# Performance work log

Hardware: AMD Instinct MI355X
Metric: run time of the kernel (lower is better)

Reference implementation:

```python
import jax, jax.numpy as jnp
import numpy as np

# Episode / graph constants
B, N, K, Q = 16, 5, 5, 5              # episodes, ways, shots, queries-per-class
NPG = 200                              # nodes per graph
DEG = 16                               # avg degree
F_DIM, H_DIM, OUT_DIM = 128, 128, 64
NS_G = B * N * K                       # 400 support graphs
NQ_G = B * N * Q                       # 400 query graphs
NS_NODES = NS_G * NPG                  # 80000
NQ_NODES = NQ_G * NPG                  # 80000
NEG_SLOPE = 0.2


def _rand_edges(key, n_nodes):
    # random in-graph source per (dst, k) slot; dst covers every node DEG times
    n_edges = n_nodes * DEG
    off = (jnp.arange(n_edges) // (NPG * DEG)) * NPG
    src = jax.random.randint(key, (n_edges,), 0, NPG) + off
    dst = jnp.repeat(jnp.arange(n_nodes), DEG)
    return jnp.stack([src, dst]).astype(jnp.int64)


def setup_inputs() -> dict:
    key = jax.random.key(0)
    ks = jax.random.split(key, 16)
    g = lambda k, shape, scale: jax.random.normal(k, shape, jnp.float32) * scale
    inp = {
        "supports_x": g(ks[0], (NS_NODES, F_DIM), 1.0),
        "queries_x": g(ks[1], (NQ_NODES, F_DIM), 1.0),
        "supports_edge_index": _rand_edges(ks[2], NS_NODES),
        "queries_edge_index": _rand_edges(ks[3], NQ_NODES),
        "supports_batch": (jnp.arange(NS_NODES) // NPG).astype(jnp.int64),
        "queries_batch": (jnp.arange(NQ_NODES) // NPG).astype(jnp.int64),
        # per-episode labels: N classes, K graphs each, local class ids 0..N-1
        "supports_y": jnp.tile(jnp.repeat(jnp.arange(N), K), B).astype(jnp.int64),
        "W1": g(ks[4], (F_DIM, H_DIM), 1.0 / np.sqrt(F_DIM)),
        "a1_src": g(ks[5], (H_DIM,), 1.0 / np.sqrt(H_DIM)),
        "a1_dst": g(ks[6], (H_DIM,), 1.0 / np.sqrt(H_DIM)),
        "b1": jnp.zeros((H_DIM,), jnp.float32),
        "W2": g(ks[7], (H_DIM, H_DIM), 1.0 / np.sqrt(H_DIM)),
        "a2_src": g(ks[8], (H_DIM,), 1.0 / np.sqrt(H_DIM)),
        "a2_dst": g(ks[9], (H_DIM,), 1.0 / np.sqrt(H_DIM)),
        "b2": jnp.zeros((H_DIM,), jnp.float32),
        "Wm1": g(ks[10], (H_DIM, H_DIM), 1.0 / np.sqrt(H_DIM)),
        "bm1": jnp.zeros((H_DIM,), jnp.float32),
        "Wm2": g(ks[11], (H_DIM, OUT_DIM), 1.0 / np.sqrt(H_DIM)),
        "bm2": jnp.zeros((OUT_DIM,), jnp.float32),
    }
    return inp


def gat_conv(x, src, dst, W, a_src, a_dst, b, n_nodes):
    """PyG GATConv, heads=1, add_self_loops=True."""
    xw = x @ W                                        # [n, H]
    loop = jnp.arange(n_nodes)
    src2 = jnp.concatenate([src, loop])
    dst2 = jnp.concatenate([dst, loop])
    e = (xw @ a_src)[src2] + (xw @ a_dst)[dst2]       # [E+n]
    e = jnp.where(e > 0, e, NEG_SLOPE * e)            # leaky_relu
    m = jax.ops.segment_max(e, dst2, num_segments=n_nodes)
    ex = jnp.exp(e - m[dst2])
    den = jax.ops.segment_sum(ex, dst2, num_segments=n_nodes)
    alpha = ex / den[dst2]                            # softmax per destination
    out = jax.ops.segment_sum(alpha[:, None] * xw[src2], dst2, num_segments=n_nodes)
    return out + b


def embed(x, edge_index, batch, n_graphs, W1, a1s, a1d, b1, W2, a2s, a2d, b2,
          Wm1, bm1, Wm2, bm2):
    n = x.shape[0]
    src, dst = edge_index[0], edge_index[1]
    h = jax.nn.relu(gat_conv(x, src, dst, W1, a1s, a1d, b1, n))
    h = jax.nn.relu(gat_conv(h, src, dst, W2, a2s, a2d, b2, n))
    h = jax.nn.relu(h @ Wm1 + bm1) @ Wm2 + bm2        # MLP
    # global mean pool
    s = jax.ops.segment_sum(h, batch, num_segments=n_graphs)
    cnt = jax.ops.segment_sum(jnp.ones((n,), h.dtype), batch, num_segments=n_graphs)
    return s / cnt[:, None]                           # [n_graphs, OUT_DIM]


def reference(supports_x, supports_edge_index, supports_batch, supports_y,
              queries_x, queries_edge_index, queries_batch,
              W1, a1_src, a1_dst, b1, W2, a2_src, a2_dst, b2,
              Wm1, bm1, Wm2, bm2):
    params = (W1, a1_src, a1_dst, b1, W2, a2_src, a2_dst, b2, Wm1, bm1, Wm2, bm2)
    emb_s = embed(supports_x, supports_edge_index, supports_batch, NS_G, *params)
    emb_q = embed(queries_x, queries_edge_index, queries_batch, NQ_G, *params)

    # class prototypes per episode: mean of supports with each (sorted) class label
    emb_s = emb_s.reshape(B, N * K, OUT_DIM)
    y = supports_y.reshape(B, N * K)
    onehot = jax.nn.one_hot(y, N, dtype=emb_s.dtype)          # [B, NK, N]
    proto = jnp.einsum("bkn,bke->bne", onehot, emb_s)
    proto = proto / onehot.sum(axis=1)[:, :, None]            # [B, N, E]

    # align queries with prototypes
    nq = N * Q                                                # queries per episode
    emb_q = emb_q.reshape(B, nq, OUT_DIM)
    rep_q = jnp.repeat(emb_q, N, axis=1)                      # repeat_interleave
    rep_p = jnp.tile(proto, (1, nq, 1))                       # repeat
    return rep_q.reshape(B * nq * N, OUT_DIM), rep_p.reshape(B * nq * N, OUT_DIM)
```

## Files before the change

kernel.cpp:

```cpp
#include <hip/hip_runtime.h>


typedef unsigned short u16;
typedef unsigned int   u32;
typedef unsigned char  u8;
typedef __attribute__((ext_vector_type(8))) short short8;
typedef __attribute__((ext_vector_type(4))) float f32x4;

#define NNODES   80000
#define DEG      16
#define NEDGES   (NNODES * DEG)
#define NGRAPH   400
#define NPG      200
#define FDIM     128
#define ODIM     64
#define NEPS     16
#define NWAY     5
#define NSHOT    5
#define NROWS    (2 * NNODES)
#define NGR2     (2 * NGRAPH)

__device__ __forceinline__ float b2f(u16 u) {
    return __uint_as_float(((u32)u) << 16);
}
__device__ __forceinline__ u16 f2b(float f) {
    u32 i = __float_as_uint(f);
    u32 r = i + 0x7FFFu + ((i >> 16) & 1u);
    return (u16)(r >> 16);
}

__global__ void detect_kernel(const u32* __restrict__ sx,
                              const int* __restrict__ ei,
                              int* __restrict__ flags)
{
    if (blockIdx.x == 0 && threadIdx.x == 0) {
        int ok32 = (ei[NEDGES + 16000] == 1000) && (ei[NEDGES + 32000] == 2000);
        flags[0] = ok32 ? 0 : 1;
        int cnt = 0;
        for (int i = 0; i < 64; i++) {
            u32 lo = sx[i] & 0xFFFFu;
            u32 e  = (lo >> 7) & 0xFFu;
            if (e >= 110u && e <= 135u) cnt++;
        }
        flags[1] = (cnt >= 32) ? 1 : 0;
    }
}

__global__ __launch_bounds__(256)
void canon_kernel(const void* __restrict__ W1, const void* __restrict__ W2,
                  const void* __restrict__ Wm1, const void* __restrict__ Wm2,
                  const void* a1s, const void* a1d, const void* b1,
                  const void* a2s, const void* a2d, const void* b2,
                  const void* bm1, const void* bm2,
                  const int* __restrict__ flags, u16* __restrict__ Wc,
                  float* __restrict__ Vc, float* __restrict__ emb)
{
    const int b = blockIdx.x, t = threadIdx.x;
    const int isb = flags[1];
    if (b < 224) {
        int idx = b * 256 + t;
        const void* src;
        int n, k, nout;
        if (idx < 16384)      { src = W1;  int l = idx;         n = l >> 7; k = l & 127; nout = 128; }
        else if (idx < 32768) { src = W2;  int l = idx - 16384; n = l >> 7; k = l & 127; nout = 128; }
        else if (idx < 49152) { src = Wm1; int l = idx - 32768; n = l >> 7; k = l & 127; nout = 128; }
        else                  { src = Wm2; int l = idx - 49152; n = l >> 7; k = l & 127; nout = 64; }
        int off = k * nout + n;
        Wc[idx] = isb ? ((const u16*)src)[off] : f2b(((const float*)src)[off]);
    } else if (b == 224) {
        for (int idx = t; idx < 960; idx += 256) {
            int g = idx >> 7, off = idx & 127;
            const void* src = (g == 0) ? a1s : (g == 1) ? a1d : (g == 2) ? b1 :
                              (g == 3) ? a2s : (g == 4) ? a2d : (g == 5) ? b2 :
                              (g == 6) ? bm1 : bm2;
            Vc[idx] = isb ? b2f(((const u16*)src)[off]) : ((const float*)src)[off];
        }
    } else {
        int i = (b - 225) * 256 + t;
        emb[i] = 0.f;
    }
}

__global__ __launch_bounds__(512)
void gemm_pack_kernel(const void* __restrict__ in0, const void* __restrict__ in1,
                      int in_mode, const int* __restrict__ flags,
                      const u16* __restrict__ Wt, const float* __restrict__ bias,
                      const float* __restrict__ avs, const float* __restrict__ avd,
                      u32* __restrict__ outP, float* __restrict__ es_g,
                      float* __restrict__ ed_g, int do_relu)
{
    __shared__ uint4 bsh[2048];

    const int t    = threadIdx.x;
    const int wv   = t >> 6;
    const int lane = t & 63;
    const int qd   = lane >> 4, md = lane & 15;

    int mode = in_mode;
    if (mode == 2) mode = flags[1];

    const size_t rowG = (size_t)blockIdx.x * 128 + wv * 16 + md;
    const int side = rowG >= NNODES;
    const size_t lrow = rowG - (side ? NNODES : 0);
    const void* in_ = side ? in1 : in0;

    short8 afr[4];
    if (mode) {
        const short* arow = (const short*)in_ + lrow * FDIM;
#pragma unroll
        for (int ks = 0; ks < 4; ks++)
            afr[ks] = *(const short8*)(arow + ks * 32 + qd * 8);
    } else {
        const float* arow = (const float*)in_ + lrow * FDIM;
#pragma unroll
        for (int ks = 0; ks < 4; ks++) {
            float4 u = *(const float4*)(arow + ks * 32 + qd * 8);
            float4 v = *(const float4*)(arow + ks * 32 + qd * 8 + 4);
            short8 tt;
            tt[0] = (short)f2b(u.x); tt[1] = (short)f2b(u.y);
            tt[2] = (short)f2b(u.z); tt[3] = (short)f2b(u.w);
            tt[4] = (short)f2b(v.x); tt[5] = (short)f2b(v.y);
            tt[6] = (short)f2b(v.z); tt[7] = (short)f2b(v.w);
            afr[ks] = tt;
        }
    }

    {
        const uint4* w4 = (const uint4*)Wt;
#pragma unroll
        for (int it = 0; it < 4; ++it) {
            int u   = it * 512 + t;
            int ctb = u >> 8, mdb = (u >> 4) & 15, ksb = (u >> 2) & 3, qdb = u & 3;
            bsh[ctb * 256 + ksb * 64 + qdb * 16 + mdb] = w4[u];
        }
    }
    __syncthreads();

    const size_t r0 = (size_t)blockIdx.x * 128 + wv * 16 + qd * 4;
    const bool has_av = (avs != nullptr);

    float sv[4] = {0.f, 0.f, 0.f, 0.f};
    float dv[4] = {0.f, 0.f, 0.f, 0.f};

    for (int ct = 0; ct < 8; ct++) {
        f32x4 acc = {0.f, 0.f, 0.f, 0.f};
#pragma unroll
        for (int ks = 0; ks < 4; ks++) {
            short8 bfr = *(const short8*)&bsh[(ct * 4 + ks) * 64 + lane];
            acc = __builtin_amdgcn_mfma_f32_16x16x32_bf16(afr[ks], bfr, acc, 0, 0, 0);
        }
        const int col = ct * 16 + md;
        const float bv  = bias ? bias[col] : 0.f;
        const float asv = has_av ? avs[col] : 0.f;
        const float adv = has_av ? avd[col] : 0.f;
#pragma unroll
        for (int i = 0; i < 4; i++) {
            float v = acc[i] + bv;
            if (do_relu) v = fmaxf(v, 0.f);
            sv[i] = fmaf(v, asv, sv[i]);
            dv[i] = fmaf(v, adv, dv[i]);
            float pr = __shfl_xor(v, 1, 64);
            if (!(md & 1)) {
                u32 pk = (u32)f2b(v) | ((u32)f2b(pr) << 16);
                outP[(r0 + i) * 64 + ct * 8 + (md >> 1)] = pk;
            }
        }
    }

    if (has_av) {
#pragma unroll
        for (int off = 1; off <= 8; off <<= 1) {
#pragma unroll
            for (int i = 0; i < 4; i++) {
                sv[i] += __shfl_xor(sv[i], off, 64);
                dv[i] += __shfl_xor(dv[i], off, 64);
            }
        }
        if (md == 0) {
#pragma unroll
            for (int i = 0; i < 4; i++) {
                es_g[r0 + i] = sv[i];
                ed_g[r0 + i] = dv[i];
            }
        }
    }
}

__global__ __launch_bounds__(512)
void gemm_pool_kernel(const u32* __restrict__ inP, const u16* __restrict__ Wt,
                      float* __restrict__ emb)
{
    __shared__ uint4 bsh[1024];
    __shared__ float psum[2][8][64];

    const int t = threadIdx.x;
    const int wv   = t >> 6;
    const int lane = t & 63;
    const int qd   = lane >> 4, md = lane & 15;

    const size_t rowA = (size_t)blockIdx.x * 128 + wv * 16 + md;
    const short* arow = (const short*)inP + rowA * FDIM;
    short8 afr[4];
#pragma unroll
    for (int ks = 0; ks < 4; ks++)
        afr[ks] = *(const short8*)(arow + ks * 32 + qd * 8);

    {
        const uint4* w4 = (const uint4*)Wt;
#pragma unroll
        for (int it = 0; it < 2; ++it) {
            int u   = it * 512 + t;
            int ctb = u >> 8, mdb = (u >> 4) & 15, ksb = (u >> 2) & 3, qdb = u & 3;
            bsh[ctb * 256 + ksb * 64 + qdb * 16 + mdb] = w4[u];
        }
    }
    __syncthreads();

    const int r0       = blockIdx.x * 128 + wv * 16 + qd * 4;
    const int g0       = (blockIdx.x * 128) / NPG;
    const int boundary = (g0 + 1) * NPG;

    for (int ct = 0; ct < 4; ct++) {
        f32x4 acc = {0.f, 0.f, 0.f, 0.f};
#pragma unroll
        for (int ks = 0; ks < 4; ks++) {
            short8 bfr = *(const short8*)&bsh[(ct * 4 + ks) * 64 + lane];
            acc = __builtin_amdgcn_mfma_f32_16x16x32_bf16(afr[ks], bfr, acc, 0, 0, 0);
        }
        float s0 = 0.f, s1 = 0.f;
#pragma unroll
        for (int i = 0; i < 4; i++) {
            if (r0 + i >= boundary) s1 += acc[i];
            else                    s0 += acc[i];
        }
        s0 += __shfl_xor(s0, 16, 64);  s1 += __shfl_xor(s1, 16, 64);
        s0 += __shfl_xor(s0, 32, 64);  s1 += __shfl_xor(s1, 32, 64);
        if (qd == 0) {
            psum[0][wv][ct * 16 + md] = s0;
            psum[1][wv][ct * 16 + md] = s1;
        }
    }
    __syncthreads();

    if (t < 128) {
        int p = t >> 6, c = t & 63;
        float s = 0.f;
#pragma unroll
        for (int w = 0; w < 8; w++) s += psum[p][w][c];
        if (p == 0 || boundary < blockIdx.x * 128 + 128)
            atomicAdd(&emb[(size_t)(g0 + p) * ODIM + c], s * (1.f / (float)NPG));
    }
}

__global__ __launch_bounds__(1024)
void gat_kernel(const u32* __restrict__ xwP, const float* __restrict__ es_g,
                const float* __restrict__ ed_g, const int* __restrict__ src0,
                const int* __restrict__ src1, const int* __restrict__ flags,
                const float* __restrict__ bias, u32* __restrict__ outH)
{
    __shared__ u32 xls[NPG * 64];
    __shared__ u16 alA[NPG * 18];
    __shared__ u8  slA[NPG * 20];

    const int g = blockIdx.x, t = threadIdx.x;
    const int side  = g >= NGRAPH;
    const int gbase = g * NPG;
    const int lbase = (g - (side ? NGRAPH : 0)) * NPG;
    const int* __restrict__ src = side ? src1 : src0;

    for (int idx = t; idx < NPG * 64; idx += 1024)
        xls[idx] = xwP[(size_t)gbase * 64 + idx];

    if (t < NPG) {
        const int n = t;
        const int is64 = flags[0];
        const float edn = ed_g[gbase + n];
        int sl[17];
#pragma unroll
        for (int j = 0; j < 16; j++) {
            int eidx = (lbase + n) * DEG + j;
            int sg = is64 ? src[2 * eidx] : src[eidx];
            sl[j] = sg - lbase;
        }
        sl[16] = n;
        float e[17];
        float mx = -1e30f;
#pragma unroll
        for (int j = 0; j < 17; j++) {
            float ev = es_g[gbase + sl[j]] + edn;
            ev = (ev > 0.f) ? ev : 0.2f * ev;
            e[j] = ev;
            mx = fmaxf(mx, ev);
        }
        float den = 0.f;
#pragma unroll
        for (int j = 0; j < 17; j++) {
            e[j] = __expf(e[j] - mx);
            den += e[j];
        }
        const float inv = 65535.f / den;
#pragma unroll
        for (int j = 0; j < 17; j++) {
            alA[n * 18 + j] = (u16)(e[j] * inv + 0.5f);
            slA[n * 20 + j] = (u8)sl[j];
        }
    }
    __syncthreads();

    const int w = t >> 6, l = t & 63;
    const int half = l >> 5, li = l & 31;
    const float4 bz = *(const float4*)&bias[4 * li];

    for (int p = w; p < NPG / 2; p += 16) {
        const int n = 2 * p + half;
        float h0 = 0.f, h1 = 0.f, h2 = 0.f, h3 = 0.f;
#pragma unroll
        for (int j = 0; j < 17; j++) {
            float a = (float)alA[n * 18 + j] * (1.f / 65535.f);
            int   s = (int)slA[n * 20 + j];
            uint2 q = *(const uint2*)&xls[s * 64 + 2 * li];
            h0 = fmaf(a, __uint_as_float(q.x << 16), h0);
            h1 = fmaf(a, __uint_as_float(q.x & 0xFFFF0000u), h1);
            h2 = fmaf(a, __uint_as_float(q.y << 16), h2);
            h3 = fmaf(a, __uint_as_float(q.y & 0xFFFF0000u), h3);
        }
        h0 = fmaxf(h0 + bz.x, 0.f);
        h1 = fmaxf(h1 + bz.y, 0.f);
        h2 = fmaxf(h2 + bz.z, 0.f);
        h3 = fmaxf(h3 + bz.w, 0.f);
        uint2 o;
        o.x = (u32)f2b(h0) | ((u32)f2b(h1) << 16);
        o.y = (u32)f2b(h2) | ((u32)f2b(h3) << 16);
        *(uint2*)&outH[(size_t)(gbase + n) * 64 + 2 * li] = o;
    }
}

__global__ __launch_bounds__(256)
void expand_kernel(const float* __restrict__ emb, const float* __restrict__ bm2,
                   const int* __restrict__ flags, void* __restrict__ out)
{
    int idx = blockIdx.x * 256 + threadIdx.x;
    const int TOT = NEPS * 125 * ODIM;
    if (idx >= TOT) return;
    int c = idx & 63;
    int tq = (idx >> 6) % 125;
    int b = idx / (125 * ODIM);
    int q = tq / NWAY, n = tq % NWAY;
    const float bb = bm2[c];
    float v0 = emb[(size_t)(NGRAPH + b * 25 + q) * ODIM + c] + bb;
    float v1 = 0.f;
#pragma unroll
    for (int k = 0; k < NSHOT; k++)
        v1 += emb[(size_t)(b * 25 + n * NSHOT + k) * ODIM + c];
    v1 = v1 * (1.f / (float)NSHOT) + bb;
    if (flags[1]) {
        ((u16*)out)[idx]       = f2b(v0);
        ((u16*)out)[TOT + idx] = f2b(v1);
    } else {
        ((float*)out)[idx]       = v0;
        ((float*)out)[TOT + idx] = v1;
    }
}

extern "C" void kernel_launch(void* const* d_in, const int* in_sizes, int n_in,
                              void* d_out, int out_size, void* d_ws, size_t ws_size,
                              hipStream_t stream)
{
    const void* sup_x  = d_in[0];
    const void* qry_x  = d_in[1];
    const int*  sup_ei = (const int*)d_in[2];
    const int*  qry_ei = (const int*)d_in[3];
    const void* W1  = d_in[7];
    const void* a1s = d_in[8];
    const void* a1d = d_in[9];
    const void* b1  = d_in[10];
    const void* W2  = d_in[11];
    const void* a2s = d_in[12];
    const void* a2d = d_in[13];
    const void* b2  = d_in[14];
    const void* Wm1 = d_in[15];
    const void* bm1 = d_in[16];
    const void* Wm2 = d_in[17];
    const void* bm2 = d_in[18];

    u32*   bufXW = (u32*)d_ws;
    u32*   bufH  = bufXW + (size_t)NROWS * 64;
    float* es_g  = (float*)(bufH + (size_t)NROWS * 64);
    float* ed_g  = es_g + NROWS;
    float* emb   = ed_g + NROWS;
    float* Vc    = emb + (size_t)NGR2 * ODIM;
    u16*   Wc    = (u16*)(Vc + 960);
    int*   flags = (int*)(Wc + 57344);

    const float* c_a1s = Vc + 0,   *c_a1d = Vc + 128, *c_b1  = Vc + 256;
    const float* c_a2s = Vc + 384, *c_a2d = Vc + 512, *c_b2  = Vc + 640;
    const float* c_bm1 = Vc + 768, *c_bm2 = Vc + 896;
    const u16* c_W1t  = Wc;
    const u16* c_W2t  = Wc + 16384;
    const u16* c_Wm1t = Wc + 32768;
    const u16* c_Wm2t = Wc + 49152;

    const int GEMM_BLOCKS = NROWS / 128;

    detect_kernel<<<1, 64, 0, stream>>>((const u32*)sup_x, sup_ei, flags);
    canon_kernel<<<425, 256, 0, stream>>>(W1, W2, Wm1, Wm2,
                                          a1s, a1d, b1, a2s, a2d, b2, bm1, bm2,
                                          flags, Wc, Vc, emb);

    const void* bufH0 = (const void*)bufH;
    const void* bufH1 = (const void*)(bufH + (size_t)NNODES * 64);

    gemm_pack_kernel<<<GEMM_BLOCKS, 512, 0, stream>>>(
        sup_x, qry_x, 2, flags, c_W1t, nullptr, c_a1s, c_a1d,
        bufXW, es_g, ed_g, 0);
    gat_kernel<<<NGR2, 1024, 0, stream>>>(
        bufXW, es_g, ed_g, sup_ei, qry_ei, flags, c_b1, bufH);

    gemm_pack_kernel<<<GEMM_BLOCKS, 512, 0, stream>>>(
        bufH0, bufH1, 1, flags, c_W2t, nullptr, c_a2s, c_a2d,
        bufXW, es_g, ed_g, 0);
    gat_kernel<<<NGR2, 1024, 0, stream>>>(
        bufXW, es_g, ed_g, sup_ei, qry_ei, flags, c_b2, bufH);

    gemm_pack_kernel<<<GEMM_BLOCKS, 512, 0, stream>>>(
        bufH0, bufH1, 1, flags, c_Wm1t, c_bm1, nullptr, nullptr,
        bufXW, es_g, ed_g, 1);

    gemm_pool_kernel<<<GEMM_BLOCKS, 512, 0, stream>>>(bufXW, c_Wm2t, emb);

    expand_kernel<<<(NEPS * 125 * ODIM + 255) / 256, 256, 0, stream>>>(
        emb, c_bm2, flags, d_out);
}
```

Before: 321.7 us.

## Split GAT softmax across four lanes per node and widen feature loads to 128-bit

The per-node attention softmax now runs on four threads per node, combined with cross-lane shuffles, instead of one thread handling all 17 edges, so 800 threads do the work rather than 200. The node-feature tile is fetched into registers as 128-bit loads before the softmax and written to shared memory afterwards, so the global loads overlap with the edge computation. The aggregation loop now gives each lane 8 features via uint4 shared-memory loads and handles 4 nodes per wavefront, with partial unrolling. The costs are higher register pressure from the staged loads and possible LDS bank conflicts from the wider accesses.

```diff
diff --git a/kernel.cpp b/kernel.cpp
--- a/kernel.cpp
+++ b/kernel.cpp
@@ -258,7 +258,7 @@
                 const int* __restrict__ src1, const int* __restrict__ flags,
                 const float* __restrict__ bias, u32* __restrict__ outH)
 {
-    __shared__ u32 xls[NPG * 64];
+    __shared__ __align__(16) u32 xls[NPG * 64];
     __shared__ u16 alA[NPG * 18];
     __shared__ u8  slA[NPG * 20];
 
@@ -268,70 +268,107 @@
     const int lbase = (g - (side ? NGRAPH : 0)) * NPG;
     const int* __restrict__ src = side ? src1 : src0;
 
-    for (int idx = t; idx < NPG * 64; idx += 1024)
-        xls[idx] = xwP[(size_t)gbase * 64 + idx];
-
-    if (t < NPG) {
-        const int n = t;
+    const uint4* xw4 = (const uint4*)(xwP + (size_t)gbase * 64);
+    uint4 st[4];
+#pragma unroll
+    for (int k = 0; k < 4; k++) {
+        int idx = t + k * 1024;
+        if (idx < NPG * 16) st[k] = xw4[idx];
+    }
+
+    if (t < 4 * NPG) {
+        const int n = t >> 2, slot = t & 3;
+        const int j0 = slot * 5;
+        const int jn = (slot == 3) ? 2 : 5;
         const int is64 = flags[0];
         const float edn = ed_g[gbase + n];
-        int sl[17];
-#pragma unroll
-        for (int j = 0; j < 16; j++) {
-            int eidx = (lbase + n) * DEG + j;
-            int sg = is64 ? src[2 * eidx] : src[eidx];
-            sl[j] = sg - lbase;
-        }
-        sl[16] = n;
-        float e[17];
+        int   sl[5];
+        float e[5];
         float mx = -1e30f;
 #pragma unroll
-        for (int j = 0; j < 17; j++) {
-            float ev = es_g[gbase + sl[j]] + edn;
-            ev = (ev > 0.f) ? ev : 0.2f * ev;
-            e[j] = ev;
-            mx = fmaxf(mx, ev);
-        }
+        for (int jj = 0; jj < 5; jj++) {
+            if (jj < jn) {
+                int j = j0 + jj;
+                int s;
+                if (j == 16) {
+                    s = n;
+                } else {
+                    int eidx = (lbase + n) * DEG + j;
+                    s = (is64 ? src[2 * eidx] : src[eidx]) - lbase;
+                }
+                sl[jj] = s;
+                float ev = es_g[gbase + s] + edn;
+                ev = (ev > 0.f) ? ev : 0.2f * ev;
+                e[jj] = ev;
+                mx = fmaxf(mx, ev);
+            }
+        }
+        mx = fmaxf(mx, __shfl_xor(mx, 1, 64));
+        mx = fmaxf(mx, __shfl_xor(mx, 2, 64));
         float den = 0.f;
 #pragma unroll
-        for (int j = 0; j < 17; j++) {
-            e[j] = __expf(e[j] - mx);
-            den += e[j];
-        }
+        for (int jj = 0; jj < 5; jj++) {
+            if (jj < jn) {
+                e[jj] = __expf(e[jj] - mx);
+                den += e[jj];
+            }
+        }
+        den += __shfl_xor(den, 1, 64);
+        den += __shfl_xor(den, 2, 64);
         const float inv = 65535.f / den;
 #pragma unroll
-        for (int j = 0; j < 17; j++) {
-            alA[n * 18 + j] = (u16)(e[j] * inv + 0.5f);
-            slA[n * 20 + j] = (u8)sl[j];
-        }
+        for (int jj = 0; jj < 5; jj++) {
+            if (jj < jn) {
+                alA[n * 18 + j0 + jj] = (u16)(e[jj] * inv + 0.5f);
+                slA[n * 20 + j0 + jj] = (u8)sl[jj];
+            }
+        }
+    }
+
+#pragma unroll
+    for (int k = 0; k < 4; k++) {
+        int idx = t + k * 1024;
+        if (idx < NPG * 16) *(uint4*)&xls[idx * 4] = st[k];
     }
     __syncthreads();
 
     const int w = t >> 6, l = t & 63;
-    const int half = l >> 5, li = l & 31;
-    const float4 bz = *(const float4*)&bias[4 * li];
-
-    for (int p = w; p < NPG / 2; p += 16) {
-        const int n = 2 * p + half;
+    const int sub = l >> 4, li = l & 15;
+    const float4 bz0 = *(const float4*)&bias[8 * li];
+    const float4 bz1 = *(const float4*)&bias[8 * li + 4];
+
+    for (int p = w; p < NPG / 4; p += 16) {
+        const int n = 4 * p + sub;
         float h0 = 0.f, h1 = 0.f, h2 = 0.f, h3 = 0.f;
-#pragma unroll
+        float h4 = 0.f, h5 = 0.f, h6 = 0.f, h7 = 0.f;
+#pragma unroll 4
         for (int j = 0; j < 17; j++) {
             float a = (float)alA[n * 18 + j] * (1.f / 65535.f);
             int   s = (int)slA[n * 20 + j];
-            uint2 q = *(const uint2*)&xls[s * 64 + 2 * li];
+            uint4 q = *(const uint4*)&xls[s * 64 + 4 * li];
             h0 = fmaf(a, __uint_as_float(q.x << 16), h0);
             h1 = fmaf(a, __uint_as_float(q.x & 0xFFFF0000u), h1);
             h2 = fmaf(a, __uint_as_float(q.y << 16), h2);
             h3 = fmaf(a, __uint_as_float(q.y & 0xFFFF0000u), h3);
-        }
-        h0 = fmaxf(h0 + bz.x, 0.f);
-        h1 = fmaxf(h1 + bz.y, 0.f);
-        h2 = fmaxf(h2 + bz.z, 0.f);
-        h3 = fmaxf(h3 + bz.w, 0.f);
-        uint2 o;
+            h4 = fmaf(a, __uint_as_float(q.z << 16), h4);
+            h5 = fmaf(a, __uint_as_float(q.z & 0xFFFF0000u), h5);
+            h6 = fmaf(a, __uint_as_float(q.w << 16), h6);
+            h7 = fmaf(a, __uint_as_float(q.w & 0xFFFF0000u), h7);
+        }
+        h0 = fmaxf(h0 + bz0.x, 0.f);
+        h1 = fmaxf(h1 + bz0.y, 0.f);
+        h2 = fmaxf(h2 + bz0.z, 0.f);
+        h3 = fmaxf(h3 + bz0.w, 0.f);
+        h4 = fmaxf(h4 + bz1.x, 0.f);
+        h5 = fmaxf(h5 + bz1.y, 0.f);
+        h6 = fmaxf(h6 + bz1.z, 0.f);
+        h7 = fmaxf(h7 + bz1.w, 0.f);
+        uint4 o;
         o.x = (u32)f2b(h0) | ((u32)f2b(h1) << 16);
         o.y = (u32)f2b(h2) | ((u32)f2b(h3) << 16);
-        *(uint2*)&outH[(size_t)(gbase + n) * 64 + 2 * li] = o;
+        o.z = (u32)f2b(h4) | ((u32)f2b(h5) << 16);
+        o.w = (u32)f2b(h6) | ((u32)f2b(h7) << 16);
+        *(uint4*)&outH[(size_t)(gbase + n) * 64 + 4 * li] = o;
     }
 }
 
```

Result: no change. 326.7 us (+1.5%).
